# Kernel tuning notes

Measured on AMD Instinct MI355X. Metric: run time of the kernel, lower is better.

The kernel has to match this reference:

```python
import jax, jax.numpy as jnp
import numpy as np

B, S, D, H = 2, 2048, 1024, 16
DK = D // H
ALPHA = 0.3


def setup_inputs() -> dict:
    key = jax.random.key(0)
    ks = jax.random.split(key, 10)
    w = 0.02  # weight init scale
    return {
        "z_real": jax.random.normal(ks[0], (B, S, D), jnp.float32),
        "z_imag": jax.random.normal(ks[1], (B, S, D), jnp.float32),
        # weights stored [in, out]; applied as x @ W (equivalent to torch Linear with weight W.T)
        "Wq_r": jax.random.normal(ks[2], (D, D), jnp.float32) * w,
        "Wq_i": jax.random.normal(ks[3], (D, D), jnp.float32) * w,
        "Wk_r": jax.random.normal(ks[4], (D, D), jnp.float32) * w,
        "Wk_i": jax.random.normal(ks[5], (D, D), jnp.float32) * w,
        "Wv": jax.random.normal(ks[6], (D, D), jnp.float32) * w,
        "Wo_w": jax.random.normal(ks[7], (D, D), jnp.float32) * w,
        "Wo_b": jnp.zeros((D,), jnp.float32),
        "mask": jax.random.randint(ks[8], (B, S), 0, 2, jnp.int32),
    }


def _heads(x):
    # [B,S,D] -> [B,S,H,DK]
    return x.reshape(B, S, H, DK)


def reference(z_real, z_imag, Wq_r, Wq_i, Wk_r, Wk_i, Wv, Wo_w, Wo_b, mask):
    scale = 1.0 / np.sqrt(DK)
    # complex projections: Q = (Wq_r + i Wq_i)(z_real + i z_imag), same for K
    Qr = _heads(z_real @ Wq_r - z_imag @ Wq_i)
    Qi = _heads(z_imag @ Wq_r + z_real @ Wq_i)
    Kr = _heads(z_real @ Wk_r - z_imag @ Wk_i)
    Ki = _heads(z_imag @ Wk_r + z_real @ Wk_i)
    V = _heads(z_real @ Wv)
    # scores = Q K^H * scale; real/imag parts without complex dtype
    Sr = (jnp.einsum('bqhd,bkhd->bhqk', Qr, Kr)
          + jnp.einsum('bqhd,bkhd->bhqk', Qi, Ki)) * scale
    Si = (jnp.einsum('bqhd,bkhd->bhqk', Qi, Kr)
          - jnp.einsum('bqhd,bkhd->bhqk', Qr, Ki)) * scale
    # variant == 'hybrid': (|s| + alpha*cos(angle(s))) / sqrt(d_k)
    mag = jnp.sqrt(Sr * Sr + Si * Si)
    cos_phase = Sr / mag  # cos(angle(s)) = Re(s)/|s|
    scores = (mag + ALPHA * cos_phase) * scale
    # key-padding mask [B,S] -> [B,1,1,S]
    scores = jnp.where(mask[:, None, None, :] == 0, -1e9, scores)
    probs = jax.nn.softmax(scores, axis=-1)  # dropout inactive (eval)
    context = jnp.einsum('bhqk,bkhd->bqhd', probs, V).reshape(B, S, D)
    out = context @ Wo_w + Wo_b
    return out, probs.mean(axis=1)
```

## Files before the change

kernel.cpp:

```cpp
#include <hip/hip_runtime.h>
#include <cstdint>
#include <cstddef>

#define BB 2
#define SS 2048
#define DD 1024
#define HH 16
#define DKK 64

typedef __attribute__((ext_vector_type(8))) short short8x;
typedef __attribute__((ext_vector_type(4))) float f32x4;

__device__ __forceinline__ unsigned short f2b(float f) {
  union { float f; unsigned u; } v; v.f = f;
  unsigned r = (v.u + 0x7fffu + ((v.u >> 16) & 1u)) >> 16;
  return (unsigned short)r;
}

__device__ __forceinline__ unsigned short f2b_fast(float f) {
  union { float f; unsigned u; } v; v.f = f;
  return (unsigned short)((v.u + 0x8000u) >> 16);
}

__device__ __forceinline__ f32x4 mfma16(short8x a, short8x b, f32x4 c) {
  return __builtin_amdgcn_mfma_f32_16x16x32_bf16(a, b, c, 0, 0, 0);
}

__device__ __forceinline__ void gload16(const unsigned short* g, unsigned short* l) {
  __builtin_amdgcn_global_load_lds(
      (__attribute__((address_space(1))) unsigned int*)g,
      (__attribute__((address_space(3))) unsigned int*)l,
      16, 0, 0);
}

#define C1F 0.0225421076f
#define C2F 0.0541010849f

__global__ __launch_bounds__(256) void pack_w_kernel(
    const float* __restrict__ Wq_r, const float* __restrict__ Wq_i,
    const float* __restrict__ Wk_r, const float* __restrict__ Wk_i,
    const float* __restrict__ Wv, const float* __restrict__ Wo,
    unsigned short* __restrict__ WcatT, unsigned short* __restrict__ WoT) {
  __shared__ float tile[64][65];
  const int tid = threadIdx.x;
  int bid = blockIdx.x;
  if (bid < 2560) {
    const int kt = bid & 31, nt = bid >> 5;
    const int k0 = kt * 64, n0 = nt * 64;
    const int q = n0 >> 10, j0 = n0 & 1023;
    const float* src;
    float sgn = 1.0f;
    bool zero = false;
    if (k0 < 1024) {
      src = (q == 0) ? Wq_r : (q == 1) ? Wq_i : (q == 2) ? Wk_r : (q == 3) ? Wk_i : Wv;
    } else {
      if (q == 0)      { src = Wq_i; sgn = -1.0f; }
      else if (q == 1) { src = Wq_r; }
      else if (q == 2) { src = Wk_i; sgn = -1.0f; }
      else if (q == 3) { src = Wk_r; }
      else             { src = Wv; zero = true; }
    }
    const int ks0 = k0 & 1023;
    if (!zero) {
#pragma unroll
      for (int i = 0; i < 16; i++) {
        int idx = i * 256 + tid;
        int r = idx >> 6, c = idx & 63;
        tile[r][c] = src[(size_t)(ks0 + r) * 1024 + j0 + c];
      }
      __syncthreads();
#pragma unroll
      for (int i = 0; i < 16; i++) {
        int idx = i * 256 + tid;
        int nr = idx >> 6, kc = idx & 63;
        WcatT[(size_t)(n0 + nr) * 2048 + k0 + kc] = f2b(sgn * tile[kc][nr]);
      }
    } else {
#pragma unroll
      for (int i = 0; i < 16; i++) {
        int idx = i * 256 + tid;
        int nr = idx >> 6, kc = idx & 63;
        WcatT[(size_t)(n0 + nr) * 2048 + k0 + kc] = 0;
      }
    }
  } else {
    bid -= 2560;
    const int kt = bid & 15, nt = bid >> 4;
    const int k0 = kt * 64, n0 = nt * 64;
#pragma unroll
    for (int i = 0; i < 16; i++) {
      int idx = i * 256 + tid;
      int r = idx >> 6, c = idx & 63;
      tile[r][c] = Wo[(size_t)(k0 + r) * 1024 + n0 + c];
    }
    __syncthreads();
#pragma unroll
    for (int i = 0; i < 16; i++) {
      int idx = i * 256 + tid;
      int nr = idx >> 6, kc = idx & 63;
      WoT[(size_t)(n0 + nr) * 1024 + k0 + kc] = f2b(tile[kc][nr]);
    }
  }
}

__global__ void pack_x_kernel(const float* __restrict__ zr, const float* __restrict__ zi,
                              unsigned short* __restrict__ X) {
  int gid = blockIdx.x * 256 + threadIdx.x;
  int k = gid & 2047, m = gid >> 11;
  float v = (k < 1024) ? zr[m * 1024 + k] : zi[m * 1024 + (k - 1024)];
  X[gid] = f2b(v);
}

__global__ void zero_kernel(float4* __restrict__ p) {
  p[(size_t)blockIdx.x * 256 + threadIdx.x] = float4{0.f, 0.f, 0.f, 0.f};
}

__global__ void mask_scan_kernel(const int* __restrict__ mask,
                                 unsigned short* __restrict__ pos,
                                 unsigned short* __restrict__ idx,
                                 int* __restrict__ cnt) {
  const int b = blockIdx.x >> 1, half = blockIdx.x & 1;
  __shared__ int sums[256];
  const int t = threadIdx.x;
  const int s0 = half * 1024 + t * 4;
  int m[4];
  int loc = 0;
#pragma unroll
  for (int i = 0; i < 4; i++) { m[i] = mask[b * 2048 + s0 + i]; loc += m[i]; }
  sums[t] = loc;
  __syncthreads();
  for (int off = 1; off < 256; off <<= 1) {
    int v = (t >= off) ? sums[t - off] : 0;
    __syncthreads();
    sums[t] += v;
    __syncthreads();
  }
  int excl = sums[t] - loc;
#pragma unroll
  for (int i = 0; i < 4; i++) {
    int sg = s0 + i;
    if (m[i]) {
      pos[b * 2048 + sg] = (unsigned short)excl;
      idx[(b * 2 + half) * 1024 + excl] = (unsigned short)sg;
      excl++;
    } else {
      pos[b * 2048 + sg] = 0xFFFFu;
    }
  }
  if (t == 255) cnt[b * 2 + half] = sums[255];
}

__global__ __launch_bounds__(256, 5) void gemm_proj_kernel(
    const unsigned short* __restrict__ A, const unsigned short* __restrict__ Bt,
    const unsigned short* __restrict__ pos,
    unsigned short* __restrict__ Qr, unsigned short* __restrict__ Qi,
    unsigned short* __restrict__ Kr, unsigned short* __restrict__ Ki,
    unsigned short* __restrict__ VT) {
  constexpr int K = 2048;
  __shared__ __attribute__((aligned(16))) unsigned short As[128][32];
  __shared__ __attribute__((aligned(16))) unsigned short Bs[128][32];
  const int tid = threadIdx.x;
  const int m0 = blockIdx.x * 128;
  const int n0 = blockIdx.y * 128;
  const int lane = tid & 63, wid = tid >> 6;
  const int l15 = lane & 15, quad = lane >> 4;
  const int wm = (wid & 1) * 64, wn = (wid >> 1) * 64;
  const int r4 = lane >> 2, c8 = (lane & 3) * 8;
  const int kmax = (n0 >= 4096) ? 1024 : K;
  f32x4 acc[4][4] = {};
  const unsigned short* pa0 = A + (size_t)(m0 + wid * 16 + r4) * K + c8;
  const unsigned short* pa1 = pa0 + (size_t)64 * K;
  const unsigned short* pb0 = Bt + (size_t)(n0 + wid * 16 + r4) * K + c8;
  const unsigned short* pb1 = pb0 + (size_t)64 * K;
  unsigned short* la0 = &As[wid * 16][0];
  unsigned short* la1 = &As[64 + wid * 16][0];
  unsigned short* lb0 = &Bs[wid * 16][0];
  unsigned short* lb1 = &Bs[64 + wid * 16][0];
  for (int k0 = 0; k0 < kmax; k0 += 32) {
    __syncthreads();
    gload16(pa0, la0);  gload16(pa1, la1);
    gload16(pb0, lb0);  gload16(pb1, lb1);
    pa0 += 32; pa1 += 32; pb0 += 32; pb1 += 32;
    __syncthreads();
    short8x af[4], bfr[4];
#pragma unroll
    for (int i = 0; i < 4; i++) af[i]  = *(const short8x*)&As[wm + i * 16 + l15][quad * 8];
#pragma unroll
    for (int i = 0; i < 4; i++) bfr[i] = *(const short8x*)&Bs[wn + i * 16 + l15][quad * 8];
#pragma unroll
    for (int mi = 0; mi < 4; mi++)
#pragma unroll
      for (int ni = 0; ni < 4; ni++)
        acc[mi][ni] = mfma16(af[mi], bfr[ni], acc[mi][ni]);
  }
#pragma unroll
  for (int mi = 0; mi < 4; mi++) {
#pragma unroll
    for (int ni = 0; ni < 4; ni++) {
      int gn = n0 + wn + ni * 16 + l15;
      if (gn < 2048) {
        int which = gn >> 10, j = gn & 1023, h = j >> 6, dk = j & 63;
        int ks = dk >> 5, q = (dk >> 3) & 3, e = dk & 7;
        unsigned short* dst = which ? Qi : Qr;
#pragma unroll
        for (int r = 0; r < 4; r++) {
          int gm = m0 + wm + mi * 16 + quad * 4 + r;
          int b = gm >> 11, s = gm & 2047;
          int bh = b * HH + h, rb = s >> 4, l = s & 15;
          dst[(size_t)(((bh * 128 + rb) * 2 + ks) * 512 + (q * 16 + l) * 8 + e)] = f2b(acc[mi][ni][r]);
        }
      } else if (gn < 4096) {
        int which = gn >> 10, j = gn & 1023, h = j >> 6, dk = j & 63;
        int ks = dk >> 5, q = (dk >> 3) & 3, e = dk & 7;
        unsigned short* dst = (which == 2) ? Kr : Ki;
#pragma unroll
        for (int r = 0; r < 4; r++) {
          int gm = m0 + wm + mi * 16 + quad * 4 + r;
          int b = gm >> 11, s = gm & 2047;
          unsigned short pp = pos[b * 2048 + s];
          if (pp != 0xFFFFu) {
            int hf = s >> 10;
            int bh = b * HH + h, rb = hf * 64 + (pp >> 4), l = pp & 15;
            dst[(size_t)(((bh * 128 + rb) * 2 + ks) * 512 + (q * 16 + l) * 8 + e)] = f2b(acc[mi][ni][r]);
          }
        }
      } else {
        int j = gn - 4096, h = j >> 6, dk = j & 63;
        int rbv = dk >> 4, lv = dk & 15;
#pragma unroll
        for (int r = 0; r < 4; r++) {
          int gm = m0 + wm + mi * 16 + quad * 4 + r;
          int b = gm >> 11, s = gm & 2047;
          unsigned short pp = pos[b * 2048 + s];
          if (pp != 0xFFFFu) {
            int hf = s >> 10;
            int bh = b * HH + h, kc = hf * 32 + (pp >> 5), qv = (pp >> 3) & 3, ev = pp & 7;
            VT[(size_t)(((bh * 4 + rbv) * 64 + kc) * 512 + (qv * 16 + lv) * 8 + ev)] = f2b(acc[mi][ni][r]);
          }
        }
      }
    }
  }
}

__global__ __launch_bounds__(256, 6) void flash_kernel(
    const unsigned short* __restrict__ Qr, const unsigned short* __restrict__ Qi,
    const unsigned short* __restrict__ Kr, const unsigned short* __restrict__ Ki,
    const unsigned short* __restrict__ VT, const int* __restrict__ cnt,
    float* __restrict__ ctxP0, float* __restrict__ ctxP1,
    float* __restrict__ Lp0, float* __restrict__ Lp1) {
  __shared__ __attribute__((aligned(16))) unsigned short Ps[4][16][72];
  const int tid = threadIdx.x;
  const int lane = tid & 63, wid = tid >> 6;
  const int l15 = lane & 15, quad = lane >> 4;
  int lin = blockIdx.x + 16 * (blockIdx.y + 16 * blockIdx.z);
  lin = ((lin & 7) << 7) | (lin >> 3);
  const int qt2 = (lin & 15) * 128;
  const int h = (lin >> 4) & 15;
  const int z = lin >> 8;
  const int b = z >> 1, half = z & 1;
  const int bh = b * HH + h;
  float* __restrict__ cp = half ? ctxP1 : ctxP0;
  float* __restrict__ lp = half ? Lp1 : Lp0;
  const int cntbh = cnt[b * 2 + half];
  const int kend = ((cntbh + 63) >> 6) << 6;
  const int kt0 = half * 1024;

#pragma unroll 1
  for (int s2 = 0; s2 < 2; s2++) {
    const int qt = qt2 + s2 * 64;
    const int rb = (qt >> 4) + wid;
    const int qbase = (bh * 128 + rb) * 1024 + lane * 8;
    short8x fqr0 = *(const short8x*)(Qr + qbase);
    short8x fqr1 = *(const short8x*)(Qr + qbase + 512);
    short8x fqi0 = *(const short8x*)(Qi + qbase);
    short8x fqi1 = *(const short8x*)(Qi + qbase + 512);
    f32x4 ctxacc[4] = {};
    float lsum[4] = {0.f, 0.f, 0.f, 0.f};

    for (int ktl = 0; ktl < kend; ktl += 64) {
      const int kt = kt0 + ktl;
#pragma unroll
      for (int nb = 0; nb < 4; nb++) {
        const int j = ktl + nb * 16 + l15;
        const int koff = (bh * 128 + (kt >> 4) + nb) * 1024 + lane * 8;
        short8x bkr0 = *(const short8x*)(Kr + koff);
        short8x bkr1 = *(const short8x*)(Kr + koff + 512);
        short8x bki0 = *(const short8x*)(Ki + koff);
        short8x bki1 = *(const short8x*)(Ki + koff + 512);
        f32x4 sr = {0.f, 0.f, 0.f, 0.f};
        sr = mfma16(fqr0, bkr0, sr);  sr = mfma16(fqr1, bkr1, sr);
        sr = mfma16(fqi0, bki0, sr);  sr = mfma16(fqi1, bki1, sr);
        f32x4 sa = {0.f, 0.f, 0.f, 0.f};
        sa = mfma16(fqi0, bkr0, sa);  sa = mfma16(fqi1, bkr1, sa);
        f32x4 sb = {0.f, 0.f, 0.f, 0.f};
        sb = mfma16(fqr0, bki0, sb);  sb = mfma16(fqr1, bki1, sb);
#pragma unroll
        for (int r = 0; r < 4; r++) {
          float a = sr[r];
          float d = sa[r] - sb[r];
          float r2 = __builtin_fmaf(a, a, d * d);
          float inv = __builtin_amdgcn_rsqf(r2);
          float arg = inv * __builtin_fmaf(C1F, r2, C2F * a);
          float p = (j < cntbh) ? __builtin_amdgcn_exp2f(arg) : 0.0f;
          lsum[r] += p;
          Ps[wid][quad * 4 + r][nb * 16 + l15] = f2b_fast(p);
        }
      }
#pragma unroll
      for (int ks = 0; ks < 2; ks++)
#pragma unroll
        for (int db = 0; db < 4; db++) {
          int voff = ((bh * 4 + db) * 64 + (kt >> 5) + ks) * 512 + lane * 8;
          short8x bv = *(const short8x*)(VT + voff);
          short8x ap = *(const short8x*)&Ps[wid][l15][ks * 32 + quad * 8];
          ctxacc[db] = mfma16(ap, bv, ctxacc[db]);
        }
    }
#pragma unroll
    for (int r = 0; r < 4; r++) {
#pragma unroll
      for (int off = 1; off < 16; off <<= 1) lsum[r] += __shfl_xor(lsum[r], off, 64);
    }
#pragma unroll
    for (int r = 0; r < 4; r++) {
      int s = qt + wid * 16 + quad * 4 + r;
#pragma unroll
      for (int db = 0; db < 4; db++)
        cp[((size_t)b * SS + s) * DD + h * DKK + db * 16 + l15] = ctxacc[db][r];
      if (l15 == 0) lp[(size_t)bh * SS + s] = lsum[r];
    }
  }
}

__global__ __launch_bounds__(256) void combine_kernel(
    const float* __restrict__ ctxP0, const float* __restrict__ ctxP1,
    const float* __restrict__ Lp0, const float* __restrict__ Lp1,
    unsigned short* __restrict__ ctx) {
  int idx = blockIdx.x * 256 + threadIdx.x;
  int g = idx * 4;
  int c = g & 1023, s = (g >> 10) & 2047, b = g >> 21;
  int h = c >> 6;
  size_t loff = (size_t)(b * HH + h) * SS + s;
  float linv = 1.0f / (Lp0[loff] + Lp1[loff]);
  float4 p0 = *(const float4*)(ctxP0 + g);
  float4 p1 = *(const float4*)(ctxP1 + g);
  ushort4 o;
  o.x = f2b((p0.x + p1.x) * linv);
  o.y = f2b((p0.y + p1.y) * linv);
  o.z = f2b((p0.z + p1.z) * linv);
  o.w = f2b((p0.w + p1.w) * linv);
  *(ushort4*)(ctx + g) = o;
}

__global__ __launch_bounds__(256, 2) void gemm_out_kernel(
    const unsigned short* __restrict__ A, const unsigned short* __restrict__ Bt,
    const float* __restrict__ bias, float* __restrict__ out) {
  constexpr int K = 1024;
  __shared__ __attribute__((aligned(16))) unsigned short As[128][32];
  __shared__ __attribute__((aligned(16))) unsigned short Bs[128][32];
  const int tid = threadIdx.x;
  const int m0 = blockIdx.x * 128;
  const int n0 = blockIdx.y * 128;
  const int lane = tid & 63, wid = tid >> 6;
  const int l15 = lane & 15, quad = lane >> 4;
  const int wm = (wid & 1) * 64, wn = (wid >> 1) * 64;
  const int r4 = lane >> 2, c8 = (lane & 3) * 8;
  f32x4 acc[4][4] = {};
  const unsigned short* pa0 = A + (size_t)(m0 + wid * 16 + r4) * K + c8;
  const unsigned short* pa1 = pa0 + (size_t)64 * K;
  const unsigned short* pb0 = Bt + (size_t)(n0 + wid * 16 + r4) * K + c8;
  const unsigned short* pb1 = pb0 + (size_t)64 * K;
  unsigned short* la0 = &As[wid * 16][0];
  unsigned short* la1 = &As[64 + wid * 16][0];
  unsigned short* lb0 = &Bs[wid * 16][0];
  unsigned short* lb1 = &Bs[64 + wid * 16][0];
  for (int k0 = 0; k0 < K; k0 += 32) {
    __syncthreads();
    gload16(pa0, la0);  gload16(pa1, la1);
    gload16(pb0, lb0);  gload16(pb1, lb1);
    pa0 += 32; pa1 += 32; pb0 += 32; pb1 += 32;
    __syncthreads();
    short8x af[4], bfr[4];
#pragma unroll
    for (int i = 0; i < 4; i++) af[i]  = *(const short8x*)&As[wm + i * 16 + l15][quad * 8];
#pragma unroll
    for (int i = 0; i < 4; i++) bfr[i] = *(const short8x*)&Bs[wn + i * 16 + l15][quad * 8];
#pragma unroll
    for (int mi = 0; mi < 4; mi++)
#pragma unroll
      for (int ni = 0; ni < 4; ni++)
        acc[mi][ni] = mfma16(af[mi], bfr[ni], acc[mi][ni]);
  }
#pragma unroll
  for (int mi = 0; mi < 4; mi++)
#pragma unroll
    for (int ni = 0; ni < 4; ni++) {
      int gn = n0 + wn + ni * 16 + l15;
      float bv = bias[gn];
#pragma unroll
      for (int r = 0; r < 4; r++) {
        int gm = m0 + wm + mi * 16 + quad * 4 + r;
        out[(size_t)gm * 1024 + gn] = acc[mi][ni][r] + bv;
      }
    }
}

__global__ __launch_bounds__(256, 4) void probsmean_kernel(
    const unsigned short* __restrict__ Qr, const unsigned short* __restrict__ Qi,
    const unsigned short* __restrict__ Kr, const unsigned short* __restrict__ Ki,
    const int* __restrict__ cnt, const unsigned short* __restrict__ idxT,
    const float* __restrict__ Lp0, const float* __restrict__ Lp1,
    float* __restrict__ out2) {
  const int tid = threadIdx.x, lane = tid & 63, wid = tid >> 6;
  const int l15 = lane & 15, quad = lane >> 4;
  const int qt = blockIdx.x * 64;
  const int b = blockIdx.z;
  const int c0 = cnt[b * 2], c1 = cnt[b * 2 + 1];
  const int t0n = (c0 + 63) >> 6;
  const int t1n = (c1 + 63) >> 6;
  const int t = blockIdx.y;
  int half, jl0, cnth;
  if (t < t0n)            { half = 0; jl0 = t * 64;         cnth = c0; }
  else if (t < t0n + t1n) { half = 1; jl0 = (t - t0n) * 64; cnth = c1; }
  else return;
  const int qrow0 = qt + wid * 16;
  const int qrb = (qt >> 4) + wid;
  const int ktb = half * 64 + (jl0 >> 4);
  int korig[4]; bool vld[4];
#pragma unroll
  for (int nb = 0; nb < 4; nb++) {
    int j = jl0 + nb * 16 + l15;
    vld[nb] = j < cnth;
    korig[nb] = idxT[(b * 2 + half) * 1024 + j];
  }
  float psum[4][4] = {};
  for (int h = 0; h < HH; h++) {
    const int bh = b * HH + h;
    const int qoff = (bh * 128 + qrb) * 1024 + lane * 8;
    short8x fqr0 = *(const short8x*)(Qr + qoff);
    short8x fqr1 = *(const short8x*)(Qr + qoff + 512);
    short8x fqi0 = *(const short8x*)(Qi + qoff);
    short8x fqi1 = *(const short8x*)(Qi + qoff + 512);
    const float4 lv0 = *(const float4*)(Lp0 + (size_t)bh * SS + qrow0 + quad * 4);
    const float4 lv1 = *(const float4*)(Lp1 + (size_t)bh * SS + qrow0 + quad * 4);
    float li[4];
    li[0] = 1.0f / (lv0.x + lv1.x); li[1] = 1.0f / (lv0.y + lv1.y);
    li[2] = 1.0f / (lv0.z + lv1.z); li[3] = 1.0f / (lv0.w + lv1.w);
#pragma unroll
    for (int nb = 0; nb < 4; nb++) {
      const int koff = (bh * 128 + ktb + nb) * 1024 + lane * 8;
      short8x bkr0 = *(const short8x*)(Kr + koff);
      short8x bkr1 = *(const short8x*)(Kr + koff + 512);
      short8x bki0 = *(const short8x*)(Ki + koff);
      short8x bki1 = *(const short8x*)(Ki + koff + 512);
      f32x4 sr = {0.f, 0.f, 0.f, 0.f};
      sr = mfma16(fqr0, bkr0, sr);  sr = mfma16(fqr1, bkr1, sr);
      sr = mfma16(fqi0, bki0, sr);  sr = mfma16(fqi1, bki1, sr);
      f32x4 sa = {0.f, 0.f, 0.f, 0.f};
      sa = mfma16(fqi0, bkr0, sa);  sa = mfma16(fqi1, bkr1, sa);
      f32x4 sb = {0.f, 0.f, 0.f, 0.f};
      sb = mfma16(fqr0, bki0, sb);  sb = mfma16(fqr1, bki1, sb);
#pragma unroll
      for (int r = 0; r < 4; r++) {
        float a = sr[r];
        float d = sa[r] - sb[r];
        float r2 = __builtin_fmaf(a, a, d * d);
        float inv = __builtin_amdgcn_rsqf(r2);
        float arg = inv * __builtin_fmaf(C1F, r2, C2F * a);
        float p = vld[nb] ? __builtin_amdgcn_exp2f(arg) * li[r] : 0.0f;
        psum[nb][r] += p;
      }
    }
  }
#pragma unroll
  for (int nb = 0; nb < 4; nb++)
#pragma unroll
    for (int r = 0; r < 4; r++) {
      if (vld[nb]) {
        int qrow = qrow0 + quad * 4 + r;
        out2[((size_t)b * SS + qrow) * SS + korig[nb]] = psum[nb][r] * 0.0625f;
      }
    }
}

extern "C" void kernel_launch(void* const* d_in, const int* in_sizes, int n_in,
                              void* d_out, int out_size, void* d_ws, size_t ws_size,
                              hipStream_t stream) {
  const float* z_real = (const float*)d_in[0];
  const float* z_imag = (const float*)d_in[1];
  const float* Wq_r = (const float*)d_in[2];
  const float* Wq_i = (const float*)d_in[3];
  const float* Wk_r = (const float*)d_in[4];
  const float* Wk_i = (const float*)d_in[5];
  const float* Wv   = (const float*)d_in[6];
  const float* Wo_w = (const float*)d_in[7];
  const float* Wo_b = (const float*)d_in[8];
  const int*   mask = (const int*)d_in[9];
  char* ws = (char*)d_ws;

  constexpr size_t QKV_BYTES = 8388608;
  unsigned short* Qr   = (unsigned short*)(ws + 0);
  unsigned short* Qi   = (unsigned short*)(ws + QKV_BYTES);
  unsigned short* Kr   = (unsigned short*)(ws + 2 * QKV_BYTES);
  unsigned short* Ki   = (unsigned short*)(ws + 3 * QKV_BYTES);
  unsigned short* VT   = (unsigned short*)(ws + 4 * QKV_BYTES);
  unsigned short* ctx  = (unsigned short*)(ws + 5 * QKV_BYTES);
  unsigned short* WcatT= (unsigned short*)(ws + 50331648);
  unsigned short* WoT  = (unsigned short*)(ws + 71303168);
  unsigned short* Xcat = (unsigned short*)(ws + 73400320);
  float* ctxP0 = (float*)(ws + 50331648);
  float* ctxP1 = (float*)(ws + 73400320);
  float* Lp0   = (float*)(ws + 90177536);
  float* Lp1   = (float*)(ws + 90439680);

  float* out  = (float*)d_out;
  float* out2 = out + (size_t)BB * SS * DD;

  unsigned short* posT = (unsigned short*)out;
  unsigned short* idxT = posT + 4096;
  int* cntT = (int*)(idxT + 4096);

  pack_w_kernel<<<dim3(2816), dim3(256), 0, stream>>>(Wq_r, Wq_i, Wk_r, Wk_i, Wv, Wo_w, WcatT, WoT);
  pack_x_kernel<<<dim3(32768), dim3(256), 0, stream>>>(z_real, z_imag, Xcat);
  zero_kernel<<<dim3(2048), dim3(256), 0, stream>>>((float4*)VT);
  zero_kernel<<<dim3(8192), dim3(256), 0, stream>>>((float4*)out2);
  mask_scan_kernel<<<dim3(4), dim3(256), 0, stream>>>(mask, posT, idxT, cntT);
  gemm_proj_kernel<<<dim3(32, 40), dim3(256), 0, stream>>>(Xcat, WcatT, posT, Qr, Qi, Kr, Ki, VT);
  flash_kernel<<<dim3(16, 16, 4), dim3(256), 0, stream>>>(Qr, Qi, Kr, Ki, VT, cntT, ctxP0, ctxP1, Lp0, Lp1);
  probsmean_kernel<<<dim3(32, 32, 2), dim3(256), 0, stream>>>(Qr, Qi, Kr, Ki, cntT, idxT, Lp0, Lp1, out2);
  combine_kernel<<<dim3(4096), dim3(256), 0, stream>>>(ctxP0, ctxP1, Lp0, Lp1, ctx);
  gemm_out_kernel<<<dim3(32, 8), dim3(256), 0, stream>>>(ctx, WoT, Wo_b, out);
}
```

Baseline: 424.3 us.

## Share K tiles across both query subtiles in flash kernel; halve out-GEMM M tile

The flash kernel now processes both 64-row query subtiles together in one pass over the keys. Each K and V fragment is loaded once and used for both, instead of sweeping the keys twice. This halves K/V global reads per block but doubles the accumulators and the P buffer in shared memory, so launch bounds drop from 6 to 4 waves. Separately, the output GEMM tile shrinks from 128 to 64 rows, doubling the grid to 512 blocks so more CUs have work.

```diff
diff --git a/kernel.cpp b/kernel.cpp
--- a/kernel.cpp
+++ b/kernel.cpp
@@ -243,13 +243,13 @@
   }
 }
 
-__global__ __launch_bounds__(256, 6) void flash_kernel(
+__global__ __launch_bounds__(256, 4) void flash_kernel(
     const unsigned short* __restrict__ Qr, const unsigned short* __restrict__ Qi,
     const unsigned short* __restrict__ Kr, const unsigned short* __restrict__ Ki,
     const unsigned short* __restrict__ VT, const int* __restrict__ cnt,
     float* __restrict__ ctxP0, float* __restrict__ ctxP1,
     float* __restrict__ Lp0, float* __restrict__ Lp1) {
-  __shared__ __attribute__((aligned(16))) unsigned short Ps[4][16][72];
+  __shared__ __attribute__((aligned(16))) unsigned short Ps[2][4][16][72];
   const int tid = threadIdx.x;
   const int lane = tid & 63, wid = tid >> 6;
   const int l15 = lane & 15, quad = lane >> 4;
@@ -266,35 +266,38 @@
   const int kend = ((cntbh + 63) >> 6) << 6;
   const int kt0 = half * 1024;
 
-#pragma unroll 1
+  short8x fqr0[2], fqr1[2], fqi0[2], fqi1[2];
+#pragma unroll
   for (int s2 = 0; s2 < 2; s2++) {
-    const int qt = qt2 + s2 * 64;
-    const int rb = (qt >> 4) + wid;
-    const int qbase = (bh * 128 + rb) * 1024 + lane * 8;
-    short8x fqr0 = *(const short8x*)(Qr + qbase);
-    short8x fqr1 = *(const short8x*)(Qr + qbase + 512);
-    short8x fqi0 = *(const short8x*)(Qi + qbase);
-    short8x fqi1 = *(const short8x*)(Qi + qbase + 512);
-    f32x4 ctxacc[4] = {};
-    float lsum[4] = {0.f, 0.f, 0.f, 0.f};
-
-    for (int ktl = 0; ktl < kend; ktl += 64) {
-      const int kt = kt0 + ktl;
-#pragma unroll
-      for (int nb = 0; nb < 4; nb++) {
-        const int j = ktl + nb * 16 + l15;
-        const int koff = (bh * 128 + (kt >> 4) + nb) * 1024 + lane * 8;
-        short8x bkr0 = *(const short8x*)(Kr + koff);
-        short8x bkr1 = *(const short8x*)(Kr + koff + 512);
-        short8x bki0 = *(const short8x*)(Ki + koff);
-        short8x bki1 = *(const short8x*)(Ki + koff + 512);
+    const int rb = ((qt2 + s2 * 64) >> 4) + wid;
+    const int qb = (bh * 128 + rb) * 1024 + lane * 8;
+    fqr0[s2] = *(const short8x*)(Qr + qb);
+    fqr1[s2] = *(const short8x*)(Qr + qb + 512);
+    fqi0[s2] = *(const short8x*)(Qi + qb);
+    fqi1[s2] = *(const short8x*)(Qi + qb + 512);
+  }
+  f32x4 ctxacc[2][4] = {};
+  float lsum[2][4] = {{0.f, 0.f, 0.f, 0.f}, {0.f, 0.f, 0.f, 0.f}};
+
+  for (int ktl = 0; ktl < kend; ktl += 64) {
+    const int kt = kt0 + ktl;
+#pragma unroll
+    for (int nb = 0; nb < 4; nb++) {
+      const int j = ktl + nb * 16 + l15;
+      const int koff = (bh * 128 + (kt >> 4) + nb) * 1024 + lane * 8;
+      short8x bkr0 = *(const short8x*)(Kr + koff);
+      short8x bkr1 = *(const short8x*)(Kr + koff + 512);
+      short8x bki0 = *(const short8x*)(Ki + koff);
+      short8x bki1 = *(const short8x*)(Ki + koff + 512);
+#pragma unroll
+      for (int s2 = 0; s2 < 2; s2++) {
         f32x4 sr = {0.f, 0.f, 0.f, 0.f};
-        sr = mfma16(fqr0, bkr0, sr);  sr = mfma16(fqr1, bkr1, sr);
-        sr = mfma16(fqi0, bki0, sr);  sr = mfma16(fqi1, bki1, sr);
+        sr = mfma16(fqr0[s2], bkr0, sr);  sr = mfma16(fqr1[s2], bkr1, sr);
+        sr = mfma16(fqi0[s2], bki0, sr);  sr = mfma16(fqi1[s2], bki1, sr);
         f32x4 sa = {0.f, 0.f, 0.f, 0.f};
-        sa = mfma16(fqi0, bkr0, sa);  sa = mfma16(fqi1, bkr1, sa);
+        sa = mfma16(fqi0[s2], bkr0, sa);  sa = mfma16(fqi1[s2], bkr1, sa);
         f32x4 sb = {0.f, 0.f, 0.f, 0.f};
-        sb = mfma16(fqr0, bki0, sb);  sb = mfma16(fqr1, bki1, sb);
+        sb = mfma16(fqr0[s2], bki0, sb);  sb = mfma16(fqr1[s2], bki1, sb);
 #pragma unroll
         for (int r = 0; r < 4; r++) {
           float a = sr[r];
@@ -303,32 +306,37 @@
           float inv = __builtin_amdgcn_rsqf(r2);
           float arg = inv * __builtin_fmaf(C1F, r2, C2F * a);
           float p = (j < cntbh) ? __builtin_amdgcn_exp2f(arg) : 0.0f;
-          lsum[r] += p;
-          Ps[wid][quad * 4 + r][nb * 16 + l15] = f2b_fast(p);
+          lsum[s2][r] += p;
+          Ps[s2][wid][quad * 4 + r][nb * 16 + l15] = f2b_fast(p);
         }
       }
-#pragma unroll
-      for (int ks = 0; ks < 2; ks++)
-#pragma unroll
-        for (int db = 0; db < 4; db++) {
-          int voff = ((bh * 4 + db) * 64 + (kt >> 5) + ks) * 512 + lane * 8;
-          short8x bv = *(const short8x*)(VT + voff);
-          short8x ap = *(const short8x*)&Ps[wid][l15][ks * 32 + quad * 8];
-          ctxacc[db] = mfma16(ap, bv, ctxacc[db]);
-        }
-    }
+    }
+#pragma unroll
+    for (int ks = 0; ks < 2; ks++)
+#pragma unroll
+      for (int db = 0; db < 4; db++) {
+        int voff = ((bh * 4 + db) * 64 + (kt >> 5) + ks) * 512 + lane * 8;
+        short8x bv = *(const short8x*)(VT + voff);
+        short8x ap0 = *(const short8x*)&Ps[0][wid][l15][ks * 32 + quad * 8];
+        short8x ap1 = *(const short8x*)&Ps[1][wid][l15][ks * 32 + quad * 8];
+        ctxacc[0][db] = mfma16(ap0, bv, ctxacc[0][db]);
+        ctxacc[1][db] = mfma16(ap1, bv, ctxacc[1][db]);
+      }
+  }
+#pragma unroll
+  for (int s2 = 0; s2 < 2; s2++) {
 #pragma unroll
     for (int r = 0; r < 4; r++) {
 #pragma unroll
-      for (int off = 1; off < 16; off <<= 1) lsum[r] += __shfl_xor(lsum[r], off, 64);
+      for (int off = 1; off < 16; off <<= 1) lsum[s2][r] += __shfl_xor(lsum[s2][r], off, 64);
     }
 #pragma unroll
     for (int r = 0; r < 4; r++) {
-      int s = qt + wid * 16 + quad * 4 + r;
+      int s = qt2 + s2 * 64 + wid * 16 + quad * 4 + r;
 #pragma unroll
       for (int db = 0; db < 4; db++)
-        cp[((size_t)b * SS + s) * DD + h * DKK + db * 16 + l15] = ctxacc[db][r];
-      if (l15 == 0) lp[(size_t)bh * SS + s] = lsum[r];
+        cp[((size_t)b * SS + s) * DD + h * DKK + db * 16 + l15] = ctxacc[s2][db][r];
+      if (l15 == 0) lp[(size_t)bh * SS + s] = lsum[s2][r];
     }
   }
 }
@@ -357,43 +365,41 @@
     const unsigned short* __restrict__ A, const unsigned short* __restrict__ Bt,
     const float* __restrict__ bias, float* __restrict__ out) {
   constexpr int K = 1024;
-  __shared__ __attribute__((aligned(16))) unsigned short As[128][32];
+  __shared__ __attribute__((aligned(16))) unsigned short As[64][32];
   __shared__ __attribute__((aligned(16))) unsigned short Bs[128][32];
   const int tid = threadIdx.x;
-  const int m0 = blockIdx.x * 128;
+  const int m0 = blockIdx.x * 64;
   const int n0 = blockIdx.y * 128;
   const int lane = tid & 63, wid = tid >> 6;
   const int l15 = lane & 15, quad = lane >> 4;
-  const int wm = (wid & 1) * 64, wn = (wid >> 1) * 64;
+  const int wm = (wid & 1) * 32, wn = (wid >> 1) * 64;
   const int r4 = lane >> 2, c8 = (lane & 3) * 8;
-  f32x4 acc[4][4] = {};
+  f32x4 acc[2][4] = {};
   const unsigned short* pa0 = A + (size_t)(m0 + wid * 16 + r4) * K + c8;
-  const unsigned short* pa1 = pa0 + (size_t)64 * K;
   const unsigned short* pb0 = Bt + (size_t)(n0 + wid * 16 + r4) * K + c8;
   const unsigned short* pb1 = pb0 + (size_t)64 * K;
   unsigned short* la0 = &As[wid * 16][0];
-  unsigned short* la1 = &As[64 + wid * 16][0];
   unsigned short* lb0 = &Bs[wid * 16][0];
   unsigned short* lb1 = &Bs[64 + wid * 16][0];
   for (int k0 = 0; k0 < K; k0 += 32) {
     __syncthreads();
-    gload16(pa0, la0);  gload16(pa1, la1);
+    gload16(pa0, la0);
     gload16(pb0, lb0);  gload16(pb1, lb1);
-    pa0 += 32; pa1 += 32; pb0 += 32; pb1 += 32;
-    __syncthreads();
-    short8x af[4], bfr[4];
-#pragma unroll
-    for (int i = 0; i < 4; i++) af[i]  = *(const short8x*)&As[wm + i * 16 + l15][quad * 8];
+    pa0 += 32; pb0 += 32; pb1 += 32;
+    __syncthreads();
+    short8x af[2], bfr[4];
+#pragma unroll
+    for (int i = 0; i < 2; i++) af[i]  = *(const short8x*)&As[wm + i * 16 + l15][quad * 8];
 #pragma unroll
     for (int i = 0; i < 4; i++) bfr[i] = *(const short8x*)&Bs[wn + i * 16 + l15][quad * 8];
 #pragma unroll
-    for (int mi = 0; mi < 4; mi++)
+    for (int mi = 0; mi < 2; mi++)
 #pragma unroll
       for (int ni = 0; ni < 4; ni++)
         acc[mi][ni] = mfma16(af[mi], bfr[ni], acc[mi][ni]);
   }
 #pragma unroll
-  for (int mi = 0; mi < 4; mi++)
+  for (int mi = 0; mi < 2; mi++)
 #pragma unroll
     for (int ni = 0; ni < 4; ni++) {
       int gn = n0 + wn + ni * 16 + l15;
@@ -530,5 +536,5 @@
   flash_kernel<<<dim3(16, 16, 4), dim3(256), 0, stream>>>(Qr, Qi, Kr, Ki, VT, cntT, ctxP0, ctxP1, Lp0, Lp1);
   probsmean_kernel<<<dim3(32, 32, 2), dim3(256), 0, stream>>>(Qr, Qi, Kr, Ki, cntT, idxT, Lp0, Lp1, out2);
   combine_kernel<<<dim3(4096), dim3(256), 0, stream>>>(ctxP0, ctxP1, Lp0, Lp1, ctx);
-  gemm_out_kernel<<<dim3(32, 8), dim3(256), 0, stream>>>(ctx, WoT, Wo_b, out);
-}
+  gemm_out_kernel<<<dim3(64, 8), dim3(256), 0, stream>>>(ctx, WoT, Wo_b, out);
+}
```

Result: faster. 404.0 us (-4.8%).
